# Kernel tuning notes

Hardware: AMD Instinct MI355X
Metric: run time of the kernel (lower is better)

Reference implementation:

```python
import jax, jax.numpy as jnp
import numpy as np

D_S = 128   # Gaussian mean dim
D_F = 1000  # feature dim
H = 4       # heads
P = 3       # render passes
V = 32000   # vocab
MAXL = 512
B, L = 4, 512


def _ln(x, g, b):
    m = jnp.mean(x, -1, keepdims=True)
    v = jnp.mean((x - m) ** 2, -1, keepdims=True)
    return (x - m) / jnp.sqrt(v + 1e-5) * g + b


def _forward(tokens, tok_mu, tok_log_var, tok_raw_alpha, tok_features, pos_mu,
             log_tau, Wq, bq, Whead, bhead, Wmu, bmu, Wg, bg, ln_g, ln_b,
             W1, b1, W2, b2, lnf_g, lnf_b, Wlm):
    Bv, Lv = tokens.shape
    mu = tok_mu[tokens] + pos_mu[:Lv][None, :, :]          # [B,L,d_s]
    log_var = tok_log_var[tokens]                          # [B,L,d_s]
    alpha = jax.nn.sigmoid(tok_raw_alpha[tokens][..., 0])  # [B,L]
    feats = tok_features[tokens]                           # [B,L,d_f]
    tau = jnp.exp(log_tau)
    mask = jnp.tril(jnp.ones((Lv, Lv), jnp.float32))       # causal [L,L]
    meaning = feats
    for p in range(P):
        # per-head queries from mu
        q = (mu @ Wq.T + bq).reshape(Bv, Lv, H, D_S).transpose(0, 2, 1, 3)  # [B,H,L,d_s]
        # factored Mahalanobis: q^2.iv - 2 q.(mu iv) + sum(mu^2 iv)
        iv = jnp.exp(-log_var)
        mu_iv = mu * iv
        mu2 = jnp.sum(mu * mu_iv, -1)                      # [B,L]
        mahal = (jnp.einsum('bhld,bjd->bhlj', q * q, iv)
                 - 2.0 * jnp.einsum('bhld,bjd->bhlj', q, mu_iv)
                 + mu2[:, None, None, :])                  # [B,H,L,L]
        K = jnp.exp(-0.5 * mahal / tau)
        # causal alpha-compositing with log-space transmittance
        eff = jnp.clip(alpha[:, None, None, :] * K * mask, 0.0, 1.0 - 1e-6)
        log_cum = jnp.cumsum(jnp.log1p(-eff), -1)
        log_T = jnp.concatenate([jnp.zeros_like(log_cum[..., :1]), log_cum[..., :-1]], -1)
        w = eff * jnp.exp(log_T)                           # [B,H,L,L]
        mh = jnp.einsum('bhlj,bjf->bhlf', w, feats)        # [B,H,L,d_f]
        meaning = mh.transpose(0, 2, 1, 3).reshape(Bv, Lv, H * D_F) @ Whead.T + bhead
        if p < P - 1:
            x = jnp.concatenate([feats, meaning], -1)      # [B,L,2*d_f]
            mu = mu + jnp.tanh(x @ Wmu[p].T + bmu[p])
            alpha = alpha * jax.nn.sigmoid(x @ Wg[p] + bg[p])
            h = _ln(x, ln_g[p], ln_b[p])
            feats = feats + (jax.nn.gelu(h @ W1[p].T + b1[p], approximate=False) @ W2[p].T + b2[p])
    y = _ln(meaning, lnf_g, lnf_b)
    return y @ Wlm.T                                       # [B,L,V]


def setup_inputs() -> dict:
    key = jax.random.key(0)
    ks = jax.random.split(key, 16)
    n = lambda k, shape, s: jax.random.normal(k, shape, jnp.float32) * s
    R = P - 1
    return {
        'tokens': jax.random.randint(ks[0], (B, L), 0, V),
        'tok_mu': n(ks[1], (V, D_S), 0.02),
        'tok_log_var': n(ks[2], (V, D_S), 0.02),
        'tok_raw_alpha': n(ks[3], (V, 1), 0.02),
        'tok_features': n(ks[4], (V, D_F), 0.02),
        'pos_mu': n(ks[5], (MAXL, D_S), 0.01),
        'log_tau': jnp.asarray(np.log(128.0), jnp.float32),
        'Wq': n(ks[6], (H * D_S, D_S), 0.02),
        'bq': jnp.zeros((H * D_S,), jnp.float32),
        'Whead': n(ks[7], (D_F, H * D_F), 0.005),
        'bhead': jnp.zeros((D_F,), jnp.float32),
        'Wmu': n(ks[8], (R, D_S, 2 * D_F), 0.02),
        'bmu': jnp.zeros((R, D_S), jnp.float32),
        'Wg': n(ks[9], (R, 2 * D_F), 0.02),
        'bg': jnp.zeros((R,), jnp.float32),
        'ln_g': jnp.ones((R, 2 * D_F), jnp.float32),
        'ln_b': jnp.zeros((R, 2 * D_F), jnp.float32),
        'W1': n(ks[10], (R, 4 * D_F, 2 * D_F), 0.02),
        'b1': jnp.zeros((R, 4 * D_F), jnp.float32),
        'W2': n(ks[11], (R, D_F, 4 * D_F), 0.02),
        'b2': jnp.zeros((R, D_F), jnp.float32),
        'lnf_g': jnp.ones((D_F,), jnp.float32),
        'lnf_b': jnp.zeros((D_F,), jnp.float32),
        'Wlm': n(ks[12], (V, D_F), 0.02),
    }


def reference(tokens, tok_mu, tok_log_var, tok_raw_alpha, tok_features, pos_mu,
              log_tau, Wq, bq, Whead, bhead, Wmu, bmu, Wg, bg, ln_g, ln_b,
              W1, b1, W2, b2, lnf_g, lnf_b, Wlm):
    return _forward(tokens, tok_mu, tok_log_var, tok_raw_alpha, tok_features,
                    pos_mu, log_tau, Wq, bq, Whead, bhead, Wmu, bmu, Wg, bg,
                    ln_g, ln_b, W1, b1, W2, b2, lnf_g, lnf_b, Wlm)
```

## Files before the change

### kernel.cpp

```cpp
#include <hip/hip_runtime.h>

#define D_S 128
#define D_F 1000
#define NH  4
#define NP  3
#define NB  4
#define SL  512
#define BL  (NB*SL)

typedef unsigned short u16;
typedef unsigned int   u32;

using short8 = __attribute__((ext_vector_type(8))) short;
using f32x4  = __attribute__((ext_vector_type(4))) float;

__global__ __launch_bounds__(256) void gather_kernel(
    const int* __restrict__ tokens, const float* __restrict__ tok_mu,
    const float* __restrict__ tok_lv, const float* __restrict__ tok_ra,
    const float* __restrict__ tok_f, const float* __restrict__ pos_mu,
    float* __restrict__ mu, float* __restrict__ iv,
    float* __restrict__ alpha, float* __restrict__ feats)
{
    int row = blockIdx.x;
    int l = row & (SL - 1);
    int tok = tokens[row];
    for (int d = threadIdx.x; d < D_S; d += 256) {
        mu[row*D_S + d] = tok_mu[tok*D_S + d] + pos_mu[l*D_S + d];
        iv[row*D_S + d] = expf(-tok_lv[tok*D_S + d]);
    }
    if (threadIdx.x == 0)
        alpha[row] = 1.f / (1.f + expf(-tok_ra[tok]));
    for (int f = threadIdx.x; f < D_F; f += 256)
        feats[row*D_F + f] = tok_f[tok*D_F + f];
}

__device__ __forceinline__ void split1(float v, u16* __restrict__ H,
                                       u16* __restrict__ L, long idx)
{
    u32 b = __float_as_uint(v);
    H[idx] = (u16)(b >> 16);
    float r = v - __uint_as_float(b & 0xffff0000u);
    u32 br = __float_as_uint(r);
    L[idx] = (u16)((br + 0x7fffu + ((br >> 16) & 1u)) >> 16);
}

__global__ __launch_bounds__(256) void split_hl(
    const float* __restrict__ src, u16* __restrict__ H, u16* __restrict__ L,
    int N, int K, int Np, int Kp)
{
    long total4 = (long)Np * Kp / 4;
    for (long i = (long)blockIdx.x * 256 + threadIdx.x; i < total4;
         i += (long)gridDim.x * 256) {
        long i4 = i * 4;
        int n = (int)(i4 / Kp);
        int k = (int)(i4 - (long)n * Kp);
        float v[4];
        if (n < N && k + 3 < K) {
            const float4 t = *(const float4*)(src + (long)n * K + k);
            v[0] = t.x; v[1] = t.y; v[2] = t.z; v[3] = t.w;
        } else {
            #pragma unroll
            for (int j = 0; j < 4; j++)
                v[j] = (n < N && k + j < K) ? src[(long)n * K + k + j] : 0.f;
        }
        u32 hh[4], ll[4];
        #pragma unroll
        for (int j = 0; j < 4; j++) {
            u32 b = __float_as_uint(v[j]);
            hh[j] = b >> 16;
            float r = v[j] - __uint_as_float(b & 0xffff0000u);
            u32 br = __float_as_uint(r);
            ll[j] = (br + 0x7fffu + ((br >> 16) & 1u)) >> 16;
        }
        uint2 hp, lp;
        hp.x = hh[0] | (hh[1] << 16); hp.y = hh[2] | (hh[3] << 16);
        lp.x = ll[0] | (ll[1] << 16); lp.y = ll[2] | (ll[3] << 16);
        *(uint2*)(H + i4) = hp;
        *(uint2*)(L + i4) = lp;
    }
}

__device__ __forceinline__ void gl_lds16(const u16* g, u16* l) {
    __builtin_amdgcn_global_load_lds(
        (const __attribute__((address_space(1))) void*)g,
        (__attribute__((address_space(3))) void*)l, 16, 0, 0);
}

template<int EPI>
__global__ __launch_bounds__(256, 2) void gemm_bf3(
    const u16* __restrict__ Ah, const u16* __restrict__ Al,
    const u16* __restrict__ Bh, const u16* __restrict__ Bl,
    const float* __restrict__ bias, float* __restrict__ C,
    int M, int N, int Kp)
{
    __shared__ u16 sAh[128*32], sAl[128*32], sBh[128*32], sBl[128*32];
    const int tid = threadIdx.x;
    const int lane = tid & 63, wid = tid >> 6;
    const int wr = wid >> 1, wc = wid & 1;

    const int nmt = gridDim.y;
    const int nwg = gridDim.x * nmt;
    const int bid = blockIdx.y * gridDim.x + blockIdx.x;
    const int work = (bid & 7) * (nwg >> 3) + (bid >> 3);
    const int bm = (work % nmt) * 128;
    const int bn = (work / nmt) * 128;

    f32x4 acc[4][4];
    const f32x4 z = {0.f, 0.f, 0.f, 0.f};
    #pragma unroll
    for (int i = 0; i < 4; i++)
        #pragma unroll
        for (int j = 0; j < 4; j++) acc[i][j] = z;

    const int nkt = Kp >> 5;
    const int kg = (lane >> 4) << 3;
    const int ar = (wr << 6) + (lane & 15);
    const int br = (wc << 6) + (lane & 15);

    for (int kt = 0; kt < nkt; ++kt) {
        const int kk = kt << 5;
        #pragma unroll
        for (int c = 0; c < 2; ++c) {
            int i   = c * 256 + tid;
            int row = i >> 2;
            int kq  = (i & 3) << 3;
            long ga = (long)(bm + row) * Kp + kk + kq;
            long gb = (long)(bn + row) * Kp + kk + kq;
            int  le = i << 3;
            gl_lds16(Ah + ga, sAh + le);
            gl_lds16(Al + ga, sAl + le);
            gl_lds16(Bh + gb, sBh + le);
            gl_lds16(Bl + gb, sBl + le);
        }
        __syncthreads();

        short8 a_h[4], a_l[4], b_h[4], b_l[4];
        #pragma unroll
        for (int t = 0; t < 4; ++t) {
            a_h[t] = *(const short8*)&sAh[(ar + t*16)*32 + kg];
            a_l[t] = *(const short8*)&sAl[(ar + t*16)*32 + kg];
            b_h[t] = *(const short8*)&sBh[(br + t*16)*32 + kg];
            b_l[t] = *(const short8*)&sBl[(br + t*16)*32 + kg];
        }
        #pragma unroll
        for (int mi = 0; mi < 4; ++mi)
            #pragma unroll
            for (int ni = 0; ni < 4; ++ni) {
                f32x4 cacc = acc[mi][ni];
                cacc = __builtin_amdgcn_mfma_f32_16x16x32_bf16(a_h[mi], b_h[ni], cacc, 0, 0, 0);
                cacc = __builtin_amdgcn_mfma_f32_16x16x32_bf16(a_l[mi], b_h[ni], cacc, 0, 0, 0);
                cacc = __builtin_amdgcn_mfma_f32_16x16x32_bf16(a_h[mi], b_l[ni], cacc, 0, 0, 0);
                acc[mi][ni] = cacc;
            }
        __syncthreads();
    }

    const int r0 = bm + (wr << 6) + ((lane >> 4) << 2);
    const int c0 = bn + (wc << 6) + (lane & 15);
    #pragma unroll
    for (int mi = 0; mi < 4; ++mi) {
        #pragma unroll
        for (int ni = 0; ni < 4; ++ni) {
            int cg = c0 + ni * 16;
            if (cg >= N) continue;
            float bv = (EPI == 0) ? 0.f : bias[cg];
            #pragma unroll
            for (int r = 0; r < 4; ++r) {
                int rg = r0 + mi * 16 + r;
                long idx = (long)rg * N + cg;
                float v = acc[mi][ni][r];
                if (EPI == 0)      C[idx] = v;
                else if (EPI == 1) C[idx] = v + bv;
                else if (EPI == 2) { float u = v + bv; C[idx] = 0.5f*u*(1.f + erff(u*0.70710678118654752f)); }
                else if (EPI == 3) C[idx] += v + bv;
                else if (EPI == 4) C[idx] += tanhf(v + bv);
            }
        }
    }
}

__global__ __launch_bounds__(256, 2) void gemm_mahal(
    const u16* __restrict__ Ah, const u16* __restrict__ Al,
    const u16* __restrict__ Bh, const u16* __restrict__ Bl,
    float* __restrict__ S)
{
    const int KP = 288;
    __shared__ u16 sAh[128*32], sAl[128*32], sBh[128*32], sBl[128*32];
    const int bmi = blockIdx.y, bni = blockIdx.x;
    if (bni > bmi) return;
    const int tid = threadIdx.x;
    const int lane = tid & 63, wid = tid >> 6;
    const int wr = wid >> 1, wc = wid & 1;
    const int bh = blockIdx.z;
    const long arow0 = (long)bh * 512 + bmi * 128;
    const long brow0 = (long)(bh >> 2) * 512 + bni * 128;

    f32x4 acc[4][4];
    const f32x4 z = {0.f, 0.f, 0.f, 0.f};
    #pragma unroll
    for (int i = 0; i < 4; i++)
        #pragma unroll
        for (int j = 0; j < 4; j++) acc[i][j] = z;

    const int kg = (lane >> 4) << 3;
    const int ar = (wr << 6) + (lane & 15);
    const int br = (wc << 6) + (lane & 15);

    for (int kt = 0; kt < 9; ++kt) {
        const int kk = kt << 5;
        #pragma unroll
        for (int c = 0; c < 2; ++c) {
            int i   = c * 256 + tid;
            int row = i >> 2;
            int kq  = (i & 3) << 3;
            long ga = (arow0 + row) * KP + kk + kq;
            long gb = (brow0 + row) * KP + kk + kq;
            int  le = i << 3;
            gl_lds16(Ah + ga, sAh + le);
            gl_lds16(Al + ga, sAl + le);
            gl_lds16(Bh + gb, sBh + le);
            gl_lds16(Bl + gb, sBl + le);
        }
        __syncthreads();
        short8 a_h[4], a_l[4], b_h[4], b_l[4];
        #pragma unroll
        for (int t = 0; t < 4; ++t) {
            a_h[t] = *(const short8*)&sAh[(ar + t*16)*32 + kg];
            a_l[t] = *(const short8*)&sAl[(ar + t*16)*32 + kg];
            b_h[t] = *(const short8*)&sBh[(br + t*16)*32 + kg];
            b_l[t] = *(const short8*)&sBl[(br + t*16)*32 + kg];
        }
        #pragma unroll
        for (int mi = 0; mi < 4; ++mi)
            #pragma unroll
            for (int ni = 0; ni < 4; ++ni) {
                f32x4 cacc = acc[mi][ni];
                cacc = __builtin_amdgcn_mfma_f32_16x16x32_bf16(a_h[mi], b_h[ni], cacc, 0, 0, 0);
                cacc = __builtin_amdgcn_mfma_f32_16x16x32_bf16(a_l[mi], b_h[ni], cacc, 0, 0, 0);
                cacc = __builtin_amdgcn_mfma_f32_16x16x32_bf16(a_h[mi], b_l[ni], cacc, 0, 0, 0);
                acc[mi][ni] = cacc;
            }
        __syncthreads();
    }

    const int r0 = bmi * 128 + (wr << 6) + ((lane >> 4) << 2);
    const int c0 = bni * 128 + (wc << 6) + (lane & 15);
    #pragma unroll
    for (int mi = 0; mi < 4; ++mi)
        #pragma unroll
        for (int ni = 0; ni < 4; ++ni) {
            int cg = c0 + ni * 16;
            #pragma unroll
            for (int r = 0; r < 4; ++r) {
                int rg = r0 + mi * 16 + r;
                S[((long)bh * 512 + rg) * 512 + cg] = acc[mi][ni][r];
            }
        }
}

__global__ __launch_bounds__(256) void build_a_ext(
    const float* __restrict__ q, u16* __restrict__ H, u16* __restrict__ L)
{
    int row = blockIdx.x;
    int bh = row >> 9, l = row & 511;
    int b = bh >> 2, h = bh & 3;
    const float* qp = q + (long)(b*SL + l)*(NH*D_S) + h*D_S;
    long base = (long)row * 288;
    for (int t = threadIdx.x; t < 288; t += 256) {
        float v;
        if (t < 128)      { float qq = qp[t]; v = qq*qq; }
        else if (t < 256)   v = qp[t-128];
        else if (t == 256)  v = 1.f;
        else                v = 0.f;
        split1(v, H, L, base + t);
    }
}

__global__ __launch_bounds__(256) void build_b_ext(
    const float* __restrict__ mu, const float* __restrict__ iv,
    u16* __restrict__ H, u16* __restrict__ L)
{
    int row = blockIdx.x;
    int tid = threadIdx.x, lane = tid & 63;
    const float* mup = mu + (long)row*D_S;
    const float* ivp = iv + (long)row*D_S;
    __shared__ float red[2];
    float part = 0.f;
    if (tid < 128) { float m = mup[tid]; part = m*m*ivp[tid]; }
    #pragma unroll
    for (int o = 32; o > 0; o >>= 1) part += __shfl_xor(part, o);
    if (tid < 128 && lane == 0) red[tid >> 6] = part;
    __syncthreads();
    float mu2 = red[0] + red[1];
    long base = (long)row * 288;
    for (int t = tid; t < 288; t += 256) {
        float v;
        if (t < 128)        v = ivp[t];
        else if (t < 256)   v = -2.f * mup[t-128] * ivp[t-128];
        else if (t == 256)  v = mu2;
        else                v = 0.f;
        split1(v, H, L, base + t);
    }
}

__global__ __launch_bounds__(256) void scan_kernel(
    float* __restrict__ S, const float* __restrict__ alpha,
    const float* __restrict__ log_tau)
{
    int row = blockIdx.x * 4 + (threadIdx.x >> 6);
    int lane = threadIdx.x & 63;
    int b = row >> 11, l = row & 511;
    float scale = -0.5f * expf(-log_tau[0]);
    long base = (long)row * 512;
    float carry = 0.f;
    for (int c = 0; c < 8; c++) {
        int j = c*64 + lane;
        float e = 0.f;
        if (j <= l) {
            float Kv = expf(scale * S[base + j]);
            e = fminf(alpha[b*SL + j] * Kv, 1.f - 1e-6f);
        }
        float le = log1pf(-e);
        float sc = le;
        #pragma unroll
        for (int o = 1; o < 64; o <<= 1) {
            float v = __shfl_up(sc, o);
            if (lane >= o) sc += v;
        }
        float logT = carry + sc - le;
        S[base + j] = e * expf(logT);
        carry += __shfl(sc, 63);
    }
}

__global__ __launch_bounds__(256) void tsplit_feats(
    const float* __restrict__ feats, u16* __restrict__ H, u16* __restrict__ L)
{
    __shared__ float tile[32][33];
    int b = blockIdx.z, f0 = blockIdx.x*32, j0 = blockIdx.y*32;
    int tx = threadIdx.x & 31, ty = threadIdx.x >> 5;
    #pragma unroll
    for (int i = 0; i < 4; i++) {
        int j = j0 + ty + 8*i, f = f0 + tx;
        tile[ty + 8*i][tx] = (f < D_F) ? feats[(long)(b*SL + j)*D_F + f] : 0.f;
    }
    __syncthreads();
    #pragma unroll
    for (int i = 0; i < 4; i++) {
        int f = f0 + ty + 8*i, j = j0 + tx;
        split1(tile[tx][ty + 8*i], H, L, ((long)(b*1024 + f))*512 + j);
    }
}

__global__ __launch_bounds__(256, 2) void gemm_mh_bf3(
    const u16* __restrict__ Ah, const u16* __restrict__ Al,
    const u16* __restrict__ Bh, const u16* __restrict__ Bl,
    float* __restrict__ mh)
{
    const int KP = 512;
    __shared__ u16 sAh[128*32], sAl[128*32], sBh[128*32], sBl[128*32];
    const int tid = threadIdx.x;
    const int lane = tid & 63, wid = tid >> 6;
    const int wr = wid >> 1, wc = wid & 1;
    const int b = blockIdx.z;
    const int bm = blockIdx.y * 128;
    const int bn = blockIdx.x * 128;
    const long arow0 = (long)b*2048 + bm;
    const long brow0 = (long)b*1024 + bn;
    const int kmax = (bm & 511) + 128;
    const int nkt = kmax >> 5;

    f32x4 acc[4][4];
    const f32x4 z = {0.f, 0.f, 0.f, 0.f};
    #pragma unroll
    for (int i = 0; i < 4; i++)
        #pragma unroll
        for (int j = 0; j < 4; j++) acc[i][j] = z;

    const int kg = (lane >> 4) << 3;
    const int ar = (wr << 6) + (lane & 15);
    const int br = (wc << 6) + (lane & 15);

    for (int kt = 0; kt < nkt; ++kt) {
        const int kk = kt << 5;
        #pragma unroll
        for (int c = 0; c < 2; ++c) {
            int i   = c * 256 + tid;
            int row = i >> 2;
            int kq  = (i & 3) << 3;
            long ga = (arow0 + row) * KP + kk + kq;
            long gb = (brow0 + row) * KP + kk + kq;
            int  le = i << 3;
            gl_lds16(Ah + ga, sAh + le);
            gl_lds16(Al + ga, sAl + le);
            gl_lds16(Bh + gb, sBh + le);
            gl_lds16(Bl + gb, sBl + le);
        }
        __syncthreads();
        short8 a_h[4], a_l[4], b_h[4], b_l[4];
        #pragma unroll
        for (int t = 0; t < 4; ++t) {
            a_h[t] = *(const short8*)&sAh[(ar + t*16)*32 + kg];
            a_l[t] = *(const short8*)&sAl[(ar + t*16)*32 + kg];
            b_h[t] = *(const short8*)&sBh[(br + t*16)*32 + kg];
            b_l[t] = *(const short8*)&sBl[(br + t*16)*32 + kg];
        }
        #pragma unroll
        for (int mi = 0; mi < 4; ++mi)
            #pragma unroll
            for (int ni = 0; ni < 4; ++ni) {
                f32x4 cacc = acc[mi][ni];
                cacc = __builtin_amdgcn_mfma_f32_16x16x32_bf16(a_h[mi], b_h[ni], cacc, 0, 0, 0);
                cacc = __builtin_amdgcn_mfma_f32_16x16x32_bf16(a_l[mi], b_h[ni], cacc, 0, 0, 0);
                cacc = __builtin_amdgcn_mfma_f32_16x16x32_bf16(a_h[mi], b_l[ni], cacc, 0, 0, 0);
                acc[mi][ni] = cacc;
            }
        __syncthreads();
    }

    const int r0 = bm + (wr << 6) + ((lane >> 4) << 2);
    const int c0 = bn + (wc << 6) + (lane & 15);
    #pragma unroll
    for (int mi = 0; mi < 4; ++mi) {
        #pragma unroll
        for (int ni = 0; ni < 4; ++ni) {
            int cg = c0 + ni * 16;
            if (cg >= D_F) continue;
            #pragma unroll
            for (int r = 0; r < 4; ++r) {
                int rg = r0 + mi * 16 + r;
                int h = rg >> 9, l = rg & 511;
                mh[((long)(b*SL + l)*NH + h)*D_F + cg] = acc[mi][ni][r];
            }
        }
    }
}

template<int EPI>
__global__ __launch_bounds__(256) void gemm_tn(
    const float* __restrict__ A, const float* __restrict__ Bt,
    const float* __restrict__ bias, float* __restrict__ C,
    int M, int N, int K)
{
    const int BM = 64, BN = 64, BK = 16;
    __shared__ float As[BK][BM + 4];
    __shared__ float Bs[BK][BN + 4];
    int tid = threadIdx.x;
    int tx = tid & 15, ty = tid >> 4;
    int bm = blockIdx.y * BM, bn = blockIdx.x * BN;
    int lr = tid >> 2;
    int lk = (tid & 3) * 4;
    float acc[4][4] = {};
    for (int kk = 0; kk < K; kk += BK) {
        int gr = bm + lr;
        int gn = bn + lr;
        #pragma unroll
        for (int i = 0; i < 4; i++) {
            int gk = kk + lk + i;
            As[lk + i][lr] = (gr < M && gk < K) ? A[(long)gr*K + gk] : 0.f;
            Bs[lk + i][lr] = (gn < N && gk < K) ? Bt[(long)gn*K + gk] : 0.f;
        }
        __syncthreads();
        #pragma unroll
        for (int k = 0; k < BK; k++) {
            float4 av = *(const float4*)&As[k][ty << 2];
            float4 bv = *(const float4*)&Bs[k][tx << 2];
            float a[4] = {av.x, av.y, av.z, av.w};
            float b[4] = {bv.x, bv.y, bv.z, bv.w};
            #pragma unroll
            for (int i = 0; i < 4; i++)
                #pragma unroll
                for (int j = 0; j < 4; j++)
                    acc[i][j] += a[i] * b[j];
        }
        __syncthreads();
    }
    #pragma unroll
    for (int i = 0; i < 4; i++) {
        int r = bm + (ty << 2) + i;
        if (r >= M) continue;
        #pragma unroll
        for (int j = 0; j < 4; j++) {
            int c = bn + (tx << 2) + j;
            if (c >= N) continue;
            float v = acc[i][j];
            long idx = (long)r*N + c;
            if (EPI == 0)      C[idx] = v;
            else if (EPI == 1) C[idx] = v + bias[c];
            else if (EPI == 2) { v += bias[c]; C[idx] = 0.5f*v*(1.f + erff(v*0.70710678118654752f)); }
            else if (EPI == 3) C[idx] += v + bias[c];
            else if (EPI == 4) C[idx] += tanhf(v + bias[c]);
        }
    }
}

__global__ __launch_bounds__(256) void gemm_mh(
    const float* __restrict__ Wfull, const float* __restrict__ feats,
    float* __restrict__ mh)
{
    const int BM = 64, BN = 64, BK = 16;
    const int M = NH*SL, N = D_F, K = SL;
    __shared__ float As[BK][BM + 4];
    __shared__ float Bs[BK][BN + 4];
    int b = blockIdx.z;
    const float* A  = Wfull + (long)b*M*K;
    const float* Bm = feats + (long)b*SL*D_F;
    int tid = threadIdx.x;
    int tx = tid & 15, ty = tid >> 4;
    int bm = blockIdx.y * BM, bn = blockIdx.x * BN;
    int kmax = (bm & (SL - 1)) + BM;
    int lrA = tid >> 2, lkA = (tid & 3) * 4;
    int lkB = tid >> 4, lnB = (tid & 15) * 4;
    float acc[4][4] = {};
    for (int kk = 0; kk < kmax; kk += BK) {
        #pragma unroll
        for (int i = 0; i < 4; i++)
            As[lkA + i][lrA] = A[(long)(bm + lrA)*K + kk + lkA + i];
        #pragma unroll
        for (int j = 0; j < 4; j++) {
            int gn = bn + lnB + j;
            Bs[lkB][lnB + j] = (gn < N) ? Bm[(long)(kk + lkB)*N + gn] : 0.f;
        }
        __syncthreads();
        #pragma unroll
        for (int k = 0; k < BK; k++) {
            float4 av = *(const float4*)&As[k][ty << 2];
            float4 bv = *(const float4*)&Bs[k][tx << 2];
            float a[4] = {av.x, av.y, av.z, av.w};
            float bb[4] = {bv.x, bv.y, bv.z, bv.w};
            #pragma unroll
            for (int i = 0; i < 4; i++)
                #pragma unroll
                for (int j = 0; j < 4; j++)
                    acc[i][j] += a[i] * bb[j];
        }
        __syncthreads();
    }
    int h = bm / SL;
    #pragma unroll
    for (int i = 0; i < 4; i++) {
        int r = bm + (ty << 2) + i;
        int l = r & (SL - 1);
        long orow = ((long)(b*SL + l)*NH + h) * D_F;
        #pragma unroll
        for (int j = 0; j < 4; j++) {
            int c = bn + (tx << 2) + j;
            if (c < N) mh[orow + c] = acc[i][j];
        }
    }
}

__global__ __launch_bounds__(256) void attn_kernel(
    const float* __restrict__ q,
    const float* __restrict__ mu,
    const float* __restrict__ iv,
    const float* __restrict__ alpha,
    const float* __restrict__ log_tau,
    float* __restrict__ wout)
{
    int l = blockIdx.x, h = blockIdx.y, b = blockIdx.z;
    int tid = threadIdx.x, lane = tid & 63, wid = tid >> 6;
    __shared__ float qs[D_S];
    __shared__ float eff_s[SL];
    float scale = -0.5f / expf(log_tau[0]);
    if (tid < D_S)
        qs[tid] = q[(long)(b*SL + l)*(NH*D_S) + h*D_S + tid];
    for (int j = tid; j < SL; j += 256) eff_s[j] = 0.f;
    __syncthreads();
    for (int j = wid; j <= l; j += 4) {
        const float* mup = mu + (long)(b*SL + j)*D_S;
        const float* ivp = iv + (long)(b*SL + j)*D_S;
        float t0 = qs[lane]      - mup[lane];
        float t1 = qs[lane + 64] - mup[lane + 64];
        float s = ivp[lane]*t0*t0 + ivp[lane + 64]*t1*t1;
        #pragma unroll
        for (int o = 32; o > 0; o >>= 1) s += __shfl_xor(s, o);
        if (lane == 0) {
            float Kv = expf(scale * s);
            float e  = fminf(alpha[b*SL + j] * Kv, 1.f - 1e-6f);
            eff_s[j] = e;
        }
    }
    __syncthreads();
    if (wid == 0) {
        float carry = 0.f;
        long orow = (((long)b*NH + h)*SL + l)*SL;
        for (int c = 0; c < SL/64; c++) {
            int j = c*64 + lane;
            float e  = eff_s[j];
            float le = log1pf(-e);
            float sc = le;
            #pragma unroll
            for (int o = 1; o < 64; o <<= 1) {
                float v = __shfl_up(sc, o);
                if (lane >= o) sc += v;
            }
            float logT = carry + sc - le;
            wout[orow + j] = e * expf(logT);
            carry += __shfl(sc, 63);
        }
    }
}

__global__ __launch_bounds__(256) void build_x(
    const float* __restrict__ feats, const float* __restrict__ meaning,
    float* __restrict__ x)
{
    long i = (long)blockIdx.x*256 + threadIdx.x;
    if (i < (long)BL*D_F) {
        int r = (int)(i / D_F), c = (int)(i % D_F);
        x[(long)r*2*D_F + c]       = feats[i];
        x[(long)r*2*D_F + D_F + c] = meaning[i];
    }
}

__global__ __launch_bounds__(256) void gate_kernel(
    const float* __restrict__ x, const float* __restrict__ Wg,
    const float* __restrict__ bg, float* __restrict__ alpha)
{
    int r = blockIdx.x;
    int tid = threadIdx.x, lane = tid & 63, wid = tid >> 6;
    float s = 0.f;
    for (int c = tid; c < 2*D_F; c += 256)
        s += x[(long)r*2*D_F + c] * Wg[c];
    #pragma unroll
    for (int o = 32; o > 0; o >>= 1) s += __shfl_xor(s, o);
    __shared__ float red[4];
    if (lane == 0) red[wid] = s;
    __syncthreads();
    if (tid == 0) {
        float t = red[0] + red[1] + red[2] + red[3] + bg[0];
        alpha[r] *= 1.f / (1.f + expf(-t));
    }
}

__global__ __launch_bounds__(256) void ln_kernel(
    const float* __restrict__ x, const float* __restrict__ g,
    const float* __restrict__ bsh, float* __restrict__ o, int D)
{
    int r = blockIdx.x;
    const float* xr = x + (long)r*D;
    int tid = threadIdx.x, lane = tid & 63, wid = tid >> 6;
    float s = 0.f, s2 = 0.f;
    for (int c = tid; c < D; c += 256) { float v = xr[c]; s += v; s2 += v*v; }
    #pragma unroll
    for (int o = 32; o > 0; o >>= 1) { s += __shfl_xor(s, o); s2 += __shfl_xor(s2, o); }
    __shared__ float rs[4], rs2[4], stat[2];
    if (lane == 0) { rs[wid] = s; rs2[wid] = s2; }
    __syncthreads();
    if (tid == 0) {
        float a = rs[0] + rs[1] + rs[2] + rs[3];
        float bb = rs2[0] + rs2[1] + rs2[2] + rs2[3];
        float mean = a / D;
        float var = bb / D - mean*mean;
        if (var < 0.f) var = 0.f;
        stat[0] = mean;
        stat[1] = 1.f / sqrtf(var + 1e-5f);
    }
    __syncthreads();
    float mean = stat[0], inv = stat[1];
    for (int c = tid; c < D; c += 256)
        o[(long)r*D + c] = (xr[c] - mean)*inv*g[c] + bsh[c];
}

extern "C" void kernel_launch(void* const* d_in, const int* in_sizes, int n_in,
                              void* d_out, int out_size, void* d_ws, size_t ws_size,
                              hipStream_t stream)
{
    const int*   tokens  = (const int*)  d_in[0];
    const float* tok_mu  = (const float*)d_in[1];
    const float* tok_lv  = (const float*)d_in[2];
    const float* tok_ra  = (const float*)d_in[3];
    const float* tok_f   = (const float*)d_in[4];
    const float* pos_mu  = (const float*)d_in[5];
    const float* log_tau = (const float*)d_in[6];
    const float* Wq      = (const float*)d_in[7];
    const float* bq      = (const float*)d_in[8];
    const float* Whead   = (const float*)d_in[9];
    const float* bhead   = (const float*)d_in[10];
    const float* Wmu     = (const float*)d_in[11];
    const float* bmu     = (const float*)d_in[12];
    const float* Wg      = (const float*)d_in[13];
    const float* bg      = (const float*)d_in[14];
    const float* ln_g    = (const float*)d_in[15];
    const float* ln_b    = (const float*)d_in[16];
    const float* W1      = (const float*)d_in[17];
    const float* b1      = (const float*)d_in[18];
    const float* W2      = (const float*)d_in[19];
    const float* b2      = (const float*)d_in[20];
    const float* lnf_g   = (const float*)d_in[21];
    const float* lnf_b   = (const float*)d_in[22];
    const float* Wlm     = (const float*)d_in[23];
    float* out = (float*)d_out;

    float* ws = (float*)d_ws;
    size_t off = 0;
    auto alloc = [&](size_t n) { float* p = ws + off; off += n; return p; };
    float* mu      = alloc((size_t)BL*D_S);
    float* iv      = alloc((size_t)BL*D_S);
    float* alpha   = alloc((size_t)BL);
    float* feats   = alloc((size_t)BL*D_F);
    float* q       = alloc((size_t)BL*NH*D_S);
    float* w       = alloc((size_t)NB*NH*SL*SL);
    float* mh      = alloc((size_t)BL*NH*D_F);
    float* meaning = alloc((size_t)BL*D_F);
    float* x       = alloc((size_t)BL*2*D_F);
    float* hbuf = w;
    float* y    = w;
    float* t    = mh;

    size_t offb = (off*sizeof(float) + 255) & ~(size_t)255;
    auto alloc16 = [&](size_t n) {
        u16* p = (u16*)((char*)d_ws + offb);
        offb = (offb + n*2 + 255) & ~(size_t)255;
        return p;
    };
    u16 *Ah     = alloc16((size_t)2048*4000), *Al     = alloc16((size_t)2048*4000);
    u16 *WqH    = alloc16((size_t)512*128),   *WqL    = alloc16((size_t)512*128);
    u16 *WheadH = alloc16((size_t)1024*4000), *WheadL = alloc16((size_t)1024*4000);
    u16 *WmuH   = alloc16((size_t)256*2016),  *WmuL   = alloc16((size_t)256*2016);
    u16 *W1H    = alloc16((size_t)2*4096*2016), *W1L  = alloc16((size_t)2*4096*2016);
    u16 *W2H    = alloc16((size_t)2*1024*4000), *W2L  = alloc16((size_t)2*1024*4000);
    u16 *WlmH   = alloc16((size_t)32000*1024),  *WlmL = alloc16((size_t)32000*1024);
    u16 *AeH    = alloc16((size_t)8192*288),  *AeL    = alloc16((size_t)8192*288);
    u16 *BeH    = alloc16((size_t)2048*288),  *BeL    = alloc16((size_t)2048*288);
    u16 *wH     = alloc16((size_t)8192*512),  *wL     = alloc16((size_t)8192*512);
    u16 *fTH    = alloc16((size_t)4*1024*512),*fTL    = alloc16((size_t)4*1024*512);
    const bool use_mfma = ws_size >= offb;

    auto SPL = [&](const float* W_, u16* H_, u16* L_, int N_, int K_, int Np_, int Kp_) {
        long t4 = (long)Np_ * Kp_ / 4;
        int nb = (int)((t4 + 255) / 256);
        if (nb > 2048) nb = 2048;
        split_hl<<<nb, 256, 0, stream>>>(W_, H_, L_, N_, K_, Np_, Kp_);
    };
    auto ASPL = [&](const float* A_, int K_, int Kp_) {
        long t4 = (long)2048 * Kp_ / 4;
        int nb = (int)((t4 + 255) / 256);
        if (nb > 2048) nb = 2048;
        split_hl<<<nb, 256, 0, stream>>>(A_, Ah, Al, 2048, K_, 2048, Kp_);
    };

    gather_kernel<<<BL, 256, 0, stream>>>(tokens, tok_mu, tok_lv, tok_ra, tok_f,
                                          pos_mu, mu, iv, alpha, feats);

    if (use_mfma) {
        SPL(Wq,    WqH,    WqL,    512,   128,  512,   128);
        SPL(Whead, WheadH, WheadL, 1000,  4000, 1024,  4000);
        SPL(Wmu,   WmuH,   WmuL,   256,   2000, 256,   2016);
        for (int p = 0; p < 2; p++) {
            SPL(W1 + (size_t)p*4000*2000, W1H + (size_t)p*4096*2016,
                W1L + (size_t)p*4096*2016, 4000, 2000, 4096, 2016);
            SPL(W2 + (size_t)p*1000*4000, W2H + (size_t)p*1024*4000,
                W2L + (size_t)p*1024*4000, 1000, 4000, 1024, 4000);
        }
        SPL(Wlm, WlmH, WlmL, 32000, 1000, 32000, 1024);

        for (int p = 0; p < NP; p++) {
            ASPL(mu, 128, 128);
            gemm_bf3<1><<<dim3(4, 16), 256, 0, stream>>>(Ah, Al, WqH, WqL, bq, q,
                                                         BL, NH*D_S, 128);
            build_a_ext<<<8192, 256, 0, stream>>>(q, AeH, AeL);
            build_b_ext<<<2048, 256, 0, stream>>>(mu, iv, BeH, BeL);
            gemm_mahal<<<dim3(4, 4, 16), 256, 0, stream>>>(AeH, AeL, BeH, BeL, w);
            scan_kernel<<<2048, 256, 0, stream>>>(w, alpha, log_tau);
            SPL(w, wH, wL, 8192, 512, 8192, 512);
            tsplit_feats<<<dim3(32, 16, NB), 256, 0, stream>>>(feats, fTH, fTL);
            gemm_mh_bf3<<<dim3(8, 16, NB), 256, 0, stream>>>(wH, wL, fTH, fTL, mh);
            ASPL(mh, 4000, 4000);
            gemm_bf3<1><<<dim3(8, 16), 256, 0, stream>>>(Ah, Al, WheadH, WheadL, bhead,
                                                         meaning, BL, D_F, 4000);
            if (p < NP - 1) {
                build_x<<<(BL*D_F + 255)/256, 256, 0, stream>>>(feats, meaning, x);
                gate_kernel<<<BL, 256, 0, stream>>>(x, Wg + (size_t)p*2*D_F, bg + p, alpha);
                ASPL(x, 2000, 2016);
                gemm_bf3<4><<<dim3(1, 16), 256, 0, stream>>>(
                    Ah, Al, WmuH + (size_t)p*128*2016, WmuL + (size_t)p*128*2016,
                    bmu + (size_t)p*D_S, mu, BL, D_S, 2016);
                ln_kernel<<<BL, 256, 0, stream>>>(x, ln_g + (size_t)p*2*D_F,
                                                  ln_b + (size_t)p*2*D_F, hbuf, 2*D_F);
                ASPL(hbuf, 2000, 2016);
                gemm_bf3<2><<<dim3(32, 16), 256, 0, stream>>>(
                    Ah, Al, W1H + (size_t)p*4096*2016, W1L + (size_t)p*4096*2016,
                    b1 + (size_t)p*4*D_F, t, BL, 4*D_F, 2016);
                ASPL(t, 4000, 4000);
                gemm_bf3<3><<<dim3(8, 16), 256, 0, stream>>>(
                    Ah, Al, W2H + (size_t)p*1024*4000, W2L + (size_t)p*1024*4000,
                    b2 + (size_t)p*D_F, feats, BL, D_F, 4000);
            }
        }
        ln_kernel<<<BL, 256, 0, stream>>>(meaning, lnf_g, lnf_b, y, D_F);
        ASPL(y, 1000, 1024);
        gemm_bf3<0><<<dim3(250, 16), 256, 0, stream>>>(Ah, Al, WlmH, WlmL, nullptr, out,
                                                       BL, 32000, 1024);
    } else {
        for (int p = 0; p < NP; p++) {
            gemm_tn<1><<<dim3(8, 32), 256, 0, stream>>>(mu, Wq, bq, q, BL, NH*D_S, D_S);
            attn_kernel<<<dim3(SL, NH, NB), 256, 0, stream>>>(q, mu, iv, alpha, log_tau, w);
            gemm_mh<<<dim3(16, 32, NB), 256, 0, stream>>>(w, feats, mh);
            gemm_tn<1><<<dim3(16, 32), 256, 0, stream>>>(mh, Whead, bhead, meaning, BL, D_F, NH*D_F);
            if (p < NP - 1) {
                build_x<<<(BL*D_F + 255)/256, 256, 0, stream>>>(feats, meaning, x);
                gate_kernel<<<BL, 256, 0, stream>>>(x, Wg + (size_t)p*2*D_F, bg + p, alpha);
                gemm_tn<4><<<dim3(2, 32), 256, 0, stream>>>(x, Wmu + (size_t)p*D_S*2*D_F,
                                                            bmu + (size_t)p*D_S, mu, BL, D_S, 2*D_F);
                ln_kernel<<<BL, 256, 0, stream>>>(x, ln_g + (size_t)p*2*D_F, ln_b + (size_t)p*2*D_F,
                                                  hbuf, 2*D_F);
                gemm_tn<2><<<dim3(63, 32), 256, 0, stream>>>(hbuf, W1 + (size_t)p*4*D_F*2*D_F,
                                                             b1 + (size_t)p*4*D_F, t, BL, 4*D_F, 2*D_F);
                gemm_tn<3><<<dim3(16, 32), 256, 0, stream>>>(t, W2 + (size_t)p*D_F*4*D_F,
                                                             b2 + (size_t)p*D_F, feats, BL, D_F, 4*D_F);
            }
        }
        ln_kernel<<<BL, 256, 0, stream>>>(meaning, lnf_g, lnf_b, y, D_F);
        gemm_tn<0><<<dim3(500, 32), 256, 0, stream>>>(y, Wlm, nullptr, out, BL, 32000, D_F);
    }
}
```

Baseline: 2.916 ms.

## Fuse bf16 hi/lo splitting into GEMM epilogues, scan, and layernorm kernels

Removes the standalone split passes by having the producers write bf16 hi/lo pairs directly: the q GEMM epilogue builds the extended Mahalanobis A operand, the scan writes split weights, the mh GEMM writes split output, and the GELU epilogue writes split activations. It also merges build_x, the gate and the layernorm into one row kernel that emits split x and h, and adds a fused final layernorm+split. This cuts float round-trips through global memory and many launches. The cost is scattered 16-bit stores from the GEMM epilogues and buffer aliasing (wH reused for h, Abig reused for several operands), which must stay ordered on the single stream.

```diff
diff --git a/kernel.cpp b/kernel.cpp
--- a/kernel.cpp
+++ b/kernel.cpp
@@ -80,6 +80,17 @@
     }
 }
 
+__global__ __launch_bounds__(256) void aext_tail(u16* __restrict__ H, u16* __restrict__ L)
+{
+    long i = (long)blockIdx.x*256 + threadIdx.x;
+    if (i < (long)8192*32) {
+        int row = (int)(i >> 5), t = (int)(i & 31);
+        long o = (long)row*288 + 256 + t;
+        H[o] = (t == 0) ? 0x3f80 : 0;
+        L[o] = 0;
+    }
+}
+
 __device__ __forceinline__ void gl_lds16(const u16* g, u16* l) {
     __builtin_amdgcn_global_load_lds(
         (const __attribute__((address_space(1))) void*)g,
@@ -91,6 +102,7 @@
     const u16* __restrict__ Ah, const u16* __restrict__ Al,
     const u16* __restrict__ Bh, const u16* __restrict__ Bl,
     const float* __restrict__ bias, float* __restrict__ C,
+    u16* __restrict__ OH, u16* __restrict__ OL,
     int M, int N, int Kp)
 {
     __shared__ u16 sAh[128*32], sAl[128*32], sBh[128*32], sBl[128*32];
@@ -171,9 +183,20 @@
                 float v = acc[mi][ni][r];
                 if (EPI == 0)      C[idx] = v;
                 else if (EPI == 1) C[idx] = v + bv;
-                else if (EPI == 2) { float u = v + bv; C[idx] = 0.5f*u*(1.f + erff(u*0.70710678118654752f)); }
                 else if (EPI == 3) C[idx] += v + bv;
                 else if (EPI == 4) C[idx] += tanhf(v + bv);
+                else if (EPI == 5) {
+                    float u = v + bv;
+                    float gl = 0.5f*u*(1.f + erff(u*0.70710678118654752f));
+                    split1(gl, OH, OL, idx);
+                }
+                else if (EPI == 6) {
+                    float qv = v + bv;
+                    int b = rg >> 9, l = rg & 511, h = cg >> 7, d = cg & 127;
+                    long base = ((long)((b << 2) | h) * 512 + l) * 288;
+                    split1(qv*qv, OH, OL, base + d);
+                    split1(qv,    OH, OL, base + 128 + d);
+                }
             }
         }
     }
@@ -258,24 +281,6 @@
         }
 }
 
-__global__ __launch_bounds__(256) void build_a_ext(
-    const float* __restrict__ q, u16* __restrict__ H, u16* __restrict__ L)
-{
-    int row = blockIdx.x;
-    int bh = row >> 9, l = row & 511;
-    int b = bh >> 2, h = bh & 3;
-    const float* qp = q + (long)(b*SL + l)*(NH*D_S) + h*D_S;
-    long base = (long)row * 288;
-    for (int t = threadIdx.x; t < 288; t += 256) {
-        float v;
-        if (t < 128)      { float qq = qp[t]; v = qq*qq; }
-        else if (t < 256)   v = qp[t-128];
-        else if (t == 256)  v = 1.f;
-        else                v = 0.f;
-        split1(v, H, L, base + t);
-    }
-}
-
 __global__ __launch_bounds__(256) void build_b_ext(
     const float* __restrict__ mu, const float* __restrict__ iv,
     u16* __restrict__ H, u16* __restrict__ L)
@@ -304,8 +309,9 @@
 }
 
 __global__ __launch_bounds__(256) void scan_kernel(
-    float* __restrict__ S, const float* __restrict__ alpha,
-    const float* __restrict__ log_tau)
+    const float* __restrict__ S, const float* __restrict__ alpha,
+    const float* __restrict__ log_tau,
+    u16* __restrict__ WH, u16* __restrict__ WL)
 {
     int row = blockIdx.x * 4 + (threadIdx.x >> 6);
     int lane = threadIdx.x & 63;
@@ -328,7 +334,7 @@
             if (lane >= o) sc += v;
         }
         float logT = carry + sc - le;
-        S[base + j] = e * expf(logT);
+        split1(e * expf(logT), WH, WL, base + j);
         carry += __shfl(sc, 63);
     }
 }
@@ -355,7 +361,7 @@
 __global__ __launch_bounds__(256, 2) void gemm_mh_bf3(
     const u16* __restrict__ Ah, const u16* __restrict__ Al,
     const u16* __restrict__ Bh, const u16* __restrict__ Bl,
-    float* __restrict__ mh)
+    u16* __restrict__ OH, u16* __restrict__ OL)
 {
     const int KP = 512;
     __shared__ u16 sAh[128*32], sAl[128*32], sBh[128*32], sBl[128*32];
@@ -430,9 +436,97 @@
             for (int r = 0; r < 4; ++r) {
                 int rg = r0 + mi * 16 + r;
                 int h = rg >> 9, l = rg & 511;
-                mh[((long)(b*SL + l)*NH + h)*D_F + cg] = acc[mi][ni][r];
+                split1(acc[mi][ni][r], OH, OL,
+                       ((long)(b*SL + l)*NH + h)*D_F + cg);
             }
         }
+    }
+}
+
+__global__ __launch_bounds__(256) void fuse_xgl(
+    const float* __restrict__ feats, const float* __restrict__ meaning,
+    const float* __restrict__ Wg, const float* __restrict__ bg,
+    float* __restrict__ alpha,
+    const float* __restrict__ g, const float* __restrict__ bsh,
+    u16* __restrict__ XH, u16* __restrict__ XL,
+    u16* __restrict__ HH, u16* __restrict__ HL)
+{
+    int r = blockIdx.x;
+    int tid = threadIdx.x, lane = tid & 63, wid = tid >> 6;
+    __shared__ float xs[2*D_F];
+    __shared__ float rd[4], rs[4], rs2[4], stat[2];
+    for (int c = tid; c < D_F; c += 256) {
+        xs[c]       = feats[(long)r*D_F + c];
+        xs[D_F + c] = meaning[(long)r*D_F + c];
+    }
+    __syncthreads();
+    float dot = 0.f, s = 0.f, s2 = 0.f;
+    for (int c = tid; c < 2*D_F; c += 256) {
+        float v = xs[c];
+        dot += v * Wg[c]; s += v; s2 += v*v;
+    }
+    #pragma unroll
+    for (int o = 32; o > 0; o >>= 1) {
+        dot += __shfl_xor(dot, o); s += __shfl_xor(s, o); s2 += __shfl_xor(s2, o);
+    }
+    if (lane == 0) { rd[wid] = dot; rs[wid] = s; rs2[wid] = s2; }
+    __syncthreads();
+    if (tid == 0) {
+        float d4 = rd[0]+rd[1]+rd[2]+rd[3] + bg[0];
+        alpha[r] *= 1.f / (1.f + expf(-d4));
+        float a  = rs[0]+rs[1]+rs[2]+rs[3];
+        float bb = rs2[0]+rs2[1]+rs2[2]+rs2[3];
+        float mean = a / (2*D_F);
+        float var = bb / (2*D_F) - mean*mean;
+        if (var < 0.f) var = 0.f;
+        stat[0] = mean;
+        stat[1] = 1.f / sqrtf(var + 1e-5f);
+    }
+    __syncthreads();
+    float mean = stat[0], inv = stat[1];
+    for (int c = tid; c < 2016; c += 256) {
+        long o = (long)r*2016 + c;
+        if (c < 2*D_F) {
+            float v = xs[c];
+            split1(v, XH, XL, o);
+            float h = (v - mean)*inv*g[c] + bsh[c];
+            split1(h, HH, HL, o);
+        } else {
+            XH[o] = 0; XL[o] = 0; HH[o] = 0; HL[o] = 0;
+        }
+    }
+}
+
+__global__ __launch_bounds__(256) void ln_split(
+    const float* __restrict__ x, const float* __restrict__ g,
+    const float* __restrict__ bsh, u16* __restrict__ OH, u16* __restrict__ OL,
+    int D, int Kp)
+{
+    int r = blockIdx.x;
+    const float* xr = x + (long)r*D;
+    int tid = threadIdx.x, lane = tid & 63, wid = tid >> 6;
+    float s = 0.f, s2 = 0.f;
+    for (int c = tid; c < D; c += 256) { float v = xr[c]; s += v; s2 += v*v; }
+    #pragma unroll
+    for (int o = 32; o > 0; o >>= 1) { s += __shfl_xor(s, o); s2 += __shfl_xor(s2, o); }
+    __shared__ float rs[4], rs2[4], stat[2];
+    if (lane == 0) { rs[wid] = s; rs2[wid] = s2; }
+    __syncthreads();
+    if (tid == 0) {
+        float a = rs[0]+rs[1]+rs[2]+rs[3];
+        float bb = rs2[0]+rs2[1]+rs2[2]+rs2[3];
+        float mean = a / D;
+        float var = bb / D - mean*mean;
+        if (var < 0.f) var = 0.f;
+        stat[0] = mean;
+        stat[1] = 1.f / sqrtf(var + 1e-5f);
+    }
+    __syncthreads();
+    float mean = stat[0], inv = stat[1];
+    for (int c = tid; c < Kp; c += 256) {
+        long o = (long)r*Kp + c;
+        if (c < D) split1((xr[c] - mean)*inv*g[c] + bsh[c], OH, OL, o);
+        else       { OH[o] = 0; OL[o] = 0; }
     }
 }
 
@@ -715,7 +809,8 @@
         offb = (offb + n*2 + 255) & ~(size_t)255;
         return p;
     };
-    u16 *Ah     = alloc16((size_t)2048*4000), *Al     = alloc16((size_t)2048*4000);
+    u16 *AbigH  = alloc16((size_t)2048*4000), *AbigL  = alloc16((size_t)2048*4000);
+    u16 *AmuH   = alloc16((size_t)2048*128),  *AmuL   = alloc16((size_t)2048*128);
     u16 *WqH    = alloc16((size_t)512*128),   *WqL    = alloc16((size_t)512*128);
     u16 *WheadH = alloc16((size_t)1024*4000), *WheadL = alloc16((size_t)1024*4000);
     u16 *WmuH   = alloc16((size_t)256*2016),  *WmuL   = alloc16((size_t)256*2016);
@@ -728,23 +823,22 @@
     u16 *fTH    = alloc16((size_t)4*1024*512),*fTL    = alloc16((size_t)4*1024*512);
     const bool use_mfma = ws_size >= offb;
 
+    u16 *XH = AbigH, *XL = AbigL;
+    u16 *HHp = wH,  *HLp = wL;
+    u16 *yH = AbigH, *yL = AbigL;
+
     auto SPL = [&](const float* W_, u16* H_, u16* L_, int N_, int K_, int Np_, int Kp_) {
         long t4 = (long)Np_ * Kp_ / 4;
         int nb = (int)((t4 + 255) / 256);
         if (nb > 2048) nb = 2048;
         split_hl<<<nb, 256, 0, stream>>>(W_, H_, L_, N_, K_, Np_, Kp_);
     };
-    auto ASPL = [&](const float* A_, int K_, int Kp_) {
-        long t4 = (long)2048 * Kp_ / 4;
-        int nb = (int)((t4 + 255) / 256);
-        if (nb > 2048) nb = 2048;
-        split_hl<<<nb, 256, 0, stream>>>(A_, Ah, Al, 2048, K_, 2048, Kp_);
-    };
 
     gather_kernel<<<BL, 256, 0, stream>>>(tokens, tok_mu, tok_lv, tok_ra, tok_f,
                                           pos_mu, mu, iv, alpha, feats);
 
     if (use_mfma) {
+        aext_tail<<<1024, 256, 0, stream>>>(AeH, AeL);
         SPL(Wq,    WqH,    WqL,    512,   128,  512,   128);
         SPL(Whead, WheadH, WheadL, 1000,  4000, 1024,  4000);
         SPL(Wmu,   WmuH,   WmuL,   256,   2000, 256,   2016);
@@ -757,42 +851,36 @@
         SPL(Wlm, WlmH, WlmL, 32000, 1000, 32000, 1024);
 
         for (int p = 0; p < NP; p++) {
-            ASPL(mu, 128, 128);
-            gemm_bf3<1><<<dim3(4, 16), 256, 0, stream>>>(Ah, Al, WqH, WqL, bq, q,
-                                                         BL, NH*D_S, 128);
-            build_a_ext<<<8192, 256, 0, stream>>>(q, AeH, AeL);
+            SPL(mu, AmuH, AmuL, 2048, 128, 2048, 128);
+            gemm_bf3<6><<<dim3(4, 16), 256, 0, stream>>>(
+                AmuH, AmuL, WqH, WqL, bq, nullptr, AeH, AeL, BL, NH*D_S, 128);
             build_b_ext<<<2048, 256, 0, stream>>>(mu, iv, BeH, BeL);
             gemm_mahal<<<dim3(4, 4, 16), 256, 0, stream>>>(AeH, AeL, BeH, BeL, w);
-            scan_kernel<<<2048, 256, 0, stream>>>(w, alpha, log_tau);
-            SPL(w, wH, wL, 8192, 512, 8192, 512);
+            scan_kernel<<<2048, 256, 0, stream>>>(w, alpha, log_tau, wH, wL);
             tsplit_feats<<<dim3(32, 16, NB), 256, 0, stream>>>(feats, fTH, fTL);
-            gemm_mh_bf3<<<dim3(8, 16, NB), 256, 0, stream>>>(wH, wL, fTH, fTL, mh);
-            ASPL(mh, 4000, 4000);
-            gemm_bf3<1><<<dim3(8, 16), 256, 0, stream>>>(Ah, Al, WheadH, WheadL, bhead,
-                                                         meaning, BL, D_F, 4000);
+            gemm_mh_bf3<<<dim3(8, 16, NB), 256, 0, stream>>>(wH, wL, fTH, fTL, AbigH, AbigL);
+            gemm_bf3<1><<<dim3(8, 16), 256, 0, stream>>>(
+                AbigH, AbigL, WheadH, WheadL, bhead, meaning, nullptr, nullptr,
+                BL, D_F, 4000);
             if (p < NP - 1) {
-                build_x<<<(BL*D_F + 255)/256, 256, 0, stream>>>(feats, meaning, x);
-                gate_kernel<<<BL, 256, 0, stream>>>(x, Wg + (size_t)p*2*D_F, bg + p, alpha);
-                ASPL(x, 2000, 2016);
+                fuse_xgl<<<BL, 256, 0, stream>>>(
+                    feats, meaning, Wg + (size_t)p*2*D_F, bg + p, alpha,
+                    ln_g + (size_t)p*2*D_F, ln_b + (size_t)p*2*D_F,
+                    XH, XL, HHp, HLp);
                 gemm_bf3<4><<<dim3(1, 16), 256, 0, stream>>>(
-                    Ah, Al, WmuH + (size_t)p*128*2016, WmuL + (size_t)p*128*2016,
-                    bmu + (size_t)p*D_S, mu, BL, D_S, 2016);
-                ln_kernel<<<BL, 256, 0, stream>>>(x, ln_g + (size_t)p*2*D_F,
-                                                  ln_b + (size_t)p*2*D_F, hbuf, 2*D_F);
-                ASPL(hbuf, 2000, 2016);
-                gemm_bf3<2><<<dim3(32, 16), 256, 0, stream>>>(
-                    Ah, Al, W1H + (size_t)p*4096*2016, W1L + (size_t)p*4096*2016,
-                    b1 + (size_t)p*4*D_F, t, BL, 4*D_F, 2016);
-                ASPL(t, 4000, 4000);
+                    XH, XL, WmuH + (size_t)p*128*2016, WmuL + (size_t)p*128*2016,
+                    bmu + (size_t)p*D_S, mu, nullptr, nullptr, BL, D_S, 2016);
+                gemm_bf3<5><<<dim3(32, 16), 256, 0, stream>>>(
+                    HHp, HLp, W1H + (size_t)p*4096*2016, W1L + (size_t)p*4096*2016,
+                    b1 + (size_t)p*4*D_F, nullptr, AbigH, AbigL, BL, 4*D_F, 2016);
                 gemm_bf3<3><<<dim3(8, 16), 256, 0, stream>>>(
-                    Ah, Al, W2H + (size_t)p*1024*4000, W2L + (size_t)p*1024*4000,
-                    b2 + (size_t)p*D_F, feats, BL, D_F, 4000);
+                    AbigH, AbigL, W2H + (size_t)p*1024*4000, W2L + (size_t)p*1024*4000,
+                    b2 + (size_t)p*D_F, feats, nullptr, nullptr, BL, D_F, 4000);
             }
         }
-        ln_kernel<<<BL, 256, 0, stream>>>(meaning, lnf_g, lnf_b, y, D_F);
-        ASPL(y, 1000, 1024);
-        gemm_bf3<0><<<dim3(250, 16), 256, 0, stream>>>(Ah, Al, WlmH, WlmL, nullptr, out,
-                                                       BL, 32000, 1024);
+        ln_split<<<BL, 256, 0, stream>>>(meaning, lnf_g, lnf_b, yH, yL, D_F, 1024);
+        gemm_bf3<0><<<dim3(250, 16), 256, 0, stream>>>(
+            yH, yL, WlmH, WlmL, nullptr, out, nullptr, nullptr, BL, 32000, 1024);
     } else {
         for (int p = 0; p < NP; p++) {
             gemm_tn<1><<<dim3(8, 32), 256, 0, stream>>>(mu, Wq, bq, q, BL, NH*D_S, D_S);
```

Result: no change. 2.903 ms (-0.4%).
